# Performance work log

Hardware: AMD Instinct MI355X
Metric: run time of the kernel (lower is better)

Reference implementation:

```python
import jax, jax.numpy as jnp
import numpy as np

K = 9          # neighbors
DIL = 1        # dilation
BN_EPS = 1e-5

def _bn(x, g, b, m, v):
    # inference batchnorm over channel (last) dim
    return (x - m) * (g * jax.lax.rsqrt(v + BN_EPS)) + b

def setup_inputs() -> dict:
    key = jax.random.key(0)
    ks = jax.random.split(key, 4)
    B, C, H, W = 8, 192, 56, 56
    Ch = 384
    s = 0.02
    return {
        'x': jax.random.normal(ks[0], (B, C, H, W), jnp.float32),
        'fc1_w': jax.random.normal(ks[1], (C, C), jnp.float32) * s,
        'fc1_b': jnp.zeros((C,), jnp.float32),
        'bn1_g': jnp.ones((C,), jnp.float32), 'bn1_b': jnp.zeros((C,), jnp.float32),
        'bn1_m': jnp.zeros((C,), jnp.float32), 'bn1_v': jnp.ones((C,), jnp.float32),
        'gc_w': jax.random.normal(ks[2], (Ch, 2 * C), jnp.float32) * s,
        'gc_b': jnp.zeros((Ch,), jnp.float32),
        'bn2_g': jnp.ones((Ch,), jnp.float32), 'bn2_b': jnp.zeros((Ch,), jnp.float32),
        'bn2_m': jnp.zeros((Ch,), jnp.float32), 'bn2_v': jnp.ones((Ch,), jnp.float32),
        'fc2_w': jax.random.normal(ks[3], (C, Ch), jnp.float32) * s,
        'fc2_b': jnp.zeros((C,), jnp.float32),
        'bn3_g': jnp.ones((C,), jnp.float32), 'bn3_b': jnp.zeros((C,), jnp.float32),
        'bn3_m': jnp.zeros((C,), jnp.float32), 'bn3_v': jnp.ones((C,), jnp.float32),
    }

def reference(x, fc1_w, fc1_b, bn1_g, bn1_b, bn1_m, bn1_v,
              gc_w, gc_b, bn2_g, bn2_b, bn2_m, bn2_v,
              fc2_w, fc2_b, bn3_g, bn3_b, bn3_m, bn3_v):
    B, C, H, W = x.shape
    N = H * W
    xf = x.reshape(B, C, N).transpose(0, 2, 1)          # (B, N, C) nodes
    shortcut = xf
    # fc1: 1x1 conv + BN
    h = _bn(jnp.einsum('bnc,oc->bno', xf, fc1_w) + fc1_b, bn1_g, bn1_b, bn1_m, bn1_v)
    # dynamic KNN on L2-normalized features (ViG dense_knn_matrix)
    hn = h / jnp.maximum(jnp.linalg.norm(h, axis=-1, keepdims=True), 1e-12)
    sim = jnp.einsum('bnc,bmc->bnm', hn, hn)            # (B, N, N) cosine sim
    _, idx = jax.lax.top_k(sim, K * DIL)                # nearest (incl. self)
    idx = idx[..., ::DIL]                               # dilated neighbors (B,N,K)
    # gather neighbor features
    x_j = jax.vmap(lambda hb, ib: hb[ib])(h, idx)       # (B, N, K, C)
    x_i = h[:, :, None, :]                              # (B, N, 1, C)
    feat = jnp.concatenate([jnp.broadcast_to(x_i, x_j.shape), x_j - x_i], axis=-1)
    # EdgeConv: conv then max over neighbors
    e = jnp.einsum('bnke,oe->bnko', feat, gc_w) + gc_b  # (B, N, K, Ch)
    m = jnp.max(e, axis=2)                              # (B, N, Ch)
    m = jax.nn.gelu(_bn(m, bn2_g, bn2_b, bn2_m, bn2_v), approximate=False)
    # fc2: 1x1 conv + BN, residual
    out = _bn(jnp.einsum('bnh,oh->bno', m, fc2_w) + fc2_b, bn3_g, bn3_b, bn3_m, bn3_v)
    out = out + shortcut
    return out.transpose(0, 2, 1).reshape(B, C, H, W)
```

## Files before the change

kernel.cpp:

```cpp
#include <hip/hip_runtime.h>

#define BDIM 256
#define NB 8
#define NC 192
#define NN 3136
#define NCH 384
#define NK 9
#define NROW (NB * NN)

typedef __attribute__((ext_vector_type(8))) short short8;
typedef __attribute__((ext_vector_type(4))) float f32x4;

__device__ __forceinline__ unsigned short f2bf(float f) {
  union { float f; unsigned u; } x{f};
  unsigned r = x.u + 0x7fff + ((x.u >> 16) & 1);
  return (unsigned short)(r >> 16);
}

__device__ __forceinline__ float bf2f(unsigned u16) {
  union { unsigned u; float f; } x{u16 << 16};
  return x.f;
}

__device__ __forceinline__ unsigned umax_(unsigned a, unsigned b) { return a > b ? a : b; }
__device__ __forceinline__ unsigned umin_(unsigned a, unsigned b) { return a < b ? a : b; }
#define UMAX3(a, b, c) umax_(umax_((a), (b)), (c))
#define CXD(x, y)                      \
  {                                    \
    unsigned h_ = umax_(x, y);         \
    unsigned l_ = umin_(x, y);         \
    x = h_;                            \
    y = l_;                            \
  }

__device__ __forceinline__ unsigned simkey(float f, unsigned it) {
  union { float f; unsigned u; } x{f + 2.0f};
  return (x.u & 0xFFFFF000u) | it;
}

__device__ __forceinline__ void gload16(const char* g, char* l) {
  __builtin_amdgcn_global_load_lds(
      (const __attribute__((address_space(1))) unsigned int*)g,
      (__attribute__((address_space(3))) unsigned int*)l, 16, 0, 0);
}

__device__ __forceinline__ void stage_tile(const char* gbase, char* lbuf, int t) {
#pragma unroll
  for (int i = 0; i < 6; ++i) {
    int L = (i * 256 + t) * 16;
    int m = L / 384;
    int kb = L - m * 384;
    gload16(gbase + m * 384 + (kb ^ ((m & 7) << 4)), lbuf + L);
  }
}

__global__ __launch_bounds__(BDIM) void k0_convw(
    const float* __restrict__ gw, const float* __restrict__ f1w,
    const float* __restrict__ f2w, unsigned short* __restrict__ gcwb,
    unsigned short* __restrict__ fc1b, unsigned short* __restrict__ fc2b) {
  int i = (blockIdx.x * BDIM + threadIdx.x) * 4;
  const float* src;
  unsigned short* dst;
  if (i < 147456) {
    int o = i / NC, k = i - o * NC;
    src = gw + (size_t)(o < NCH ? o : o - NCH) * (2 * NC) + (o < NCH ? 0 : NC) + k;
    dst = gcwb + i;
  } else if (i < 184320) {
    int j = i - 147456;
    src = f1w + j;
    dst = fc1b + j;
  } else {
    int j = i - 184320;
    int o = j / NCH, k = j - o * NCH;
    int oc = o >> 6, om = o & 63;
    int kh = k / 192, km = k - kh * 192;
    src = f2w + j;
    dst = fc2b + ((size_t)((oc * 2 + kh) * 64 + om)) * 192 + km;
  }
  float4 v = *(const float4*)src;
  uint2 u;
  u.x = (unsigned)f2bf(v.x) | ((unsigned)f2bf(v.y) << 16);
  u.y = (unsigned)f2bf(v.z) | ((unsigned)f2bf(v.w) << 16);
  *(uint2*)dst = u;
}

__global__ __launch_bounds__(384) void k0b_params(
    const float* __restrict__ f1b, const float* __restrict__ g1,
    const float* __restrict__ b1, const float* __restrict__ m1,
    const float* __restrict__ v1, const float* __restrict__ gcb,
    const float* __restrict__ g2, const float* __restrict__ b2,
    const float* __restrict__ m2, const float* __restrict__ v2,
    const float* __restrict__ f2b, const float* __restrict__ g3,
    const float* __restrict__ b3, const float* __restrict__ m3,
    const float* __restrict__ v3, float* __restrict__ sc1,
    float* __restrict__ sh1, float* __restrict__ sc2, float* __restrict__ sh2,
    float* __restrict__ sc3, float* __restrict__ sh3) {
  int c = threadIdx.x;
  if (c < NC) {
    float s1 = g1[c] * rsqrtf(v1[c] + 1e-5f);
    sc1[c] = s1;
    sh1[c] = (f1b[c] - m1[c]) * s1 + b1[c];
    float s3 = g3[c] * rsqrtf(v3[c] + 1e-5f);
    sc3[c] = s3;
    sh3[c] = (f2b[c] - m3[c]) * s3 + b3[c];
  }
  float s2 = g2[c] * rsqrtf(v2[c] + 1e-5f);
  sc2[c] = s2;
  sh2[c] = (gcb[c] - m2[c]) * s2 + b2[c];
}

__global__ __launch_bounds__(BDIM) void k1_mfma(
    const float* __restrict__ x, const unsigned short* __restrict__ fc1b,
    const float* __restrict__ sc1, const float* __restrict__ sh1,
    unsigned short* __restrict__ hnb, float* __restrict__ normo) {
  __shared__ __align__(16) char abuf[2][24576];
  int t = threadIdx.x;
  int b = blockIdx.x / 49, n0 = (blockIdx.x % 49) * 64;
  int lane = t & 63, w = t >> 6;
  int l15 = lane & 15, l4 = lane >> 4;
  int n = n0 + w * 16 + l15;
  short8 bfr[6];
  {
    const float* xcol = x + (size_t)b * NC * NN + n;
#pragma unroll
    for (int ks = 0; ks < 6; ++ks) {
      union { short8 s; unsigned u[4]; } pk;
#pragma unroll
      for (int j = 0; j < 4; ++j) {
        float v0 = xcol[(size_t)(ks * 32 + l4 * 8 + 2 * j) * NN];
        float v1 = xcol[(size_t)(ks * 32 + l4 * 8 + 2 * j + 1) * NN];
        pk.u[j] = (unsigned)f2bf(v0) | ((unsigned)f2bf(v1) << 16);
      }
      bfr[ks] = pk.s;
    }
  }
  f32x4 acc[3][4];
#pragma unroll
  for (int oc = 0; oc < 3; ++oc)
#pragma unroll
    for (int sub = 0; sub < 4; ++sub) acc[oc][sub] = {0.f, 0.f, 0.f, 0.f};

  const char* wB = (const char*)fc1b;
  stage_tile(wB, abuf[0], t);
  __syncthreads();
  for (int oc = 0; oc < 3; ++oc) {
    int cur = oc & 1;
    if (oc < 2) stage_tile(wB + (size_t)(oc + 1) * 24576, abuf[cur ^ 1], t);
#pragma unroll
    for (int sub = 0; sub < 4; ++sub) {
      int r_ = sub * 16 + l15;
      int rbase = r_ * 384, sw = (r_ & 7) << 4;
#pragma unroll
      for (int ks = 0; ks < 6; ++ks) {
        short8 af = *(const short8*)&abuf[cur][rbase + ((ks * 64 + l4 * 16) ^ sw)];
        acc[oc][sub] = __builtin_amdgcn_mfma_f32_16x16x32_bf16(af, bfr[ks],
                                                               acc[oc][sub], 0, 0, 0);
      }
    }
    __syncthreads();
  }
  float p = 0.f;
#pragma unroll
  for (int oc = 0; oc < 3; ++oc)
#pragma unroll
    for (int sub = 0; sub < 4; ++sub) {
      int c4 = oc * 64 + sub * 16 + l4 * 4;
      float s_[4], h_[4];
      *(float4*)s_ = *(const float4*)&sc1[c4];
      *(float4*)h_ = *(const float4*)&sh1[c4];
#pragma unroll
      for (int r = 0; r < 4; ++r) {
        float v = acc[oc][sub][r] * s_[r] + h_[r];
        acc[oc][sub][r] = v;
        p += v * v;
      }
    }
  p += __shfl_xor(p, 16);
  p += __shfl_xor(p, 32);
  float nr = fmaxf(sqrtf(p), 1e-12f);
  float iv = 1.f / nr;
  if (l4 == 0) normo[(size_t)b * NN + n] = nr;
#pragma unroll
  for (int oc = 0; oc < 3; ++oc)
#pragma unroll
    for (int sub = 0; sub < 4; ++sub) {
      uint2 u;
      u.x = (unsigned)f2bf(acc[oc][sub][0] * iv) |
            ((unsigned)f2bf(acc[oc][sub][1] * iv) << 16);
      u.y = (unsigned)f2bf(acc[oc][sub][2] * iv) |
            ((unsigned)f2bf(acc[oc][sub][3] * iv) << 16);
      *(uint2*)&hnb[(size_t)(b * NN + n) * NC + oc * 64 + sub * 16 + l4 * 4] = u;
    }
}

__global__ __launch_bounds__(512) void k23_fused(
    const unsigned short* __restrict__ hnb, const float* __restrict__ norm,
    const unsigned short* __restrict__ gcwb, unsigned* __restrict__ candK,
    unsigned short* __restrict__ P, unsigned short* __restrict__ Q) {
  __shared__ __align__(16) char abuf[3][12288];
  int t = threadIdx.x;
  int bid = blockIdx.x;
  int b = bid & 7;
  int j = bid >> 3;
  int lane = t & 63, w = t >> 6;
  int l15 = lane & 15, l4 = lane >> 4;
  int wg = w & 3, sub = w >> 2;
  const unsigned short* hb = hnb + (size_t)b * NN * NC;

  int LA = t * 16;
  int mA = LA / 384, kbA = LA - mA * 384;
  int gA = mA * 384 + (kbA ^ ((mA & 7) << 4));
  int LB = (384 + t) * 16;
  int mB = LB / 384, kbB = LB - mB * 384;
  int gB = mB * 384 + (kbB ^ ((mB & 7) << 4));
  bool stg = (t < 384);
  int r_ = sub * 16 + l15;
  int rbase = r_ * 384, sw = (r_ & 7) << 4;
  int dso[6];
#pragma unroll
  for (int ks = 0; ks < 6; ++ks) dso[ks] = rbase + ((ks * 64 + l4 * 16) ^ sw);

  if (j % 5 != 4) {
    int idx2a = (j / 5) * 4 + (j % 5);
    int n0 = (idx2a >> 2) * 64;
    int seg = idx2a & 3;
    int mt0 = (98 * seg) / 4, mt1 = (98 * (seg + 1)) / 4;
    const char* hbB = (const char*)hb;

    short8 bfr[6];
    {
      const short8* brow =
          (const short8*)(hb + (size_t)(n0 + wg * 16 + l15) * NC + l4 * 8);
#pragma unroll
      for (int ks = 0; ks < 6; ++ks) bfr[ks] = brow[ks * 4];
    }
    unsigned tk[NK];
#pragma unroll
    for (int r = 0; r < NK; ++r) tk[r] = 0u;

    {
      const char* src = hbB + (size_t)mt0 * 12288;
      if (stg) { gload16(src + gA, abuf[0] + LA); gload16(src + gB, abuf[0] + LB); }
    }
    int nt = mt1 - mt0;
    int cur = 0;
    for (int ti = 0; ti < nt; ++ti) {
      int nxt = cur + 1 == 3 ? 0 : cur + 1;
      if (ti + 1 < nt) {
        const char* src = hbB + (size_t)(mt0 + ti + 1) * 12288;
        char* dl = &abuf[nxt][0];
        if (stg) { gload16(src + gA, dl + LA); gload16(src + gB, dl + LB); }
        asm volatile("s_waitcnt vmcnt(2)" ::: "memory");
      } else {
        asm volatile("s_waitcnt vmcnt(0)" ::: "memory");
      }
      __builtin_amdgcn_s_barrier();
      __builtin_amdgcn_sched_barrier(0);
      const char* lb = &abuf[cur][0];
      short8 af[6];
#pragma unroll
      for (int ks = 0; ks < 6; ++ks) af[ks] = *(const short8*)&lb[dso[ks]];
      f32x4 acc = {0.f, 0.f, 0.f, 0.f};
#pragma unroll
      for (int ks = 0; ks < 6; ++ks)
        acc = __builtin_amdgcn_mfma_f32_16x16x32_bf16(af[ks], bfr[ks], acc, 0, 0, 0);
      unsigned mknd = (unsigned)(4095 - ((mt0 + ti) * 32 + sub * 16 + l4 * 4));
      unsigned c0 = simkey(acc[0], mknd);
      unsigned c1 = simkey(acc[1], mknd - 1);
      unsigned c2 = simkey(acc[2], mknd - 2);
      unsigned c3 = simkey(acc[3], mknd - 3);
      CXD(c0, c1); CXD(c2, c3); CXD(c0, c2); CXD(c1, c3); CXD(c1, c2);
      tk[8] = UMAX3(UMAX3(tk[8], umin_(tk[7], c0), umin_(tk[6], c1)),
                    umin_(tk[5], c2), umin_(tk[4], c3));
      tk[7] = UMAX3(UMAX3(tk[7], umin_(tk[6], c0), umin_(tk[5], c1)),
                    umin_(tk[4], c2), umin_(tk[3], c3));
      tk[6] = UMAX3(UMAX3(tk[6], umin_(tk[5], c0), umin_(tk[4], c1)),
                    umin_(tk[3], c2), umin_(tk[2], c3));
      tk[5] = UMAX3(UMAX3(tk[5], umin_(tk[4], c0), umin_(tk[3], c1)),
                    umin_(tk[2], c2), umin_(tk[1], c3));
      tk[4] = UMAX3(UMAX3(tk[4], umin_(tk[3], c0), umin_(tk[2], c1)),
                    umin_(tk[1], c2), umin_(tk[0], c3));
      tk[3] = UMAX3(UMAX3(tk[3], c3, umin_(tk[2], c0)),
                    umin_(tk[1], c1), umin_(tk[0], c2));
      tk[2] = umax_(UMAX3(tk[2], c2, umin_(tk[1], c0)), umin_(tk[0], c1));
      tk[1] = UMAX3(tk[1], c1, umin_(tk[0], c0));
      tk[0] = umax_(tk[0], c0);
      cur = nxt;
    }
    __syncthreads();
    unsigned* mkeys = (unsigned*)&abuf[0][0];
    int rw = wg * 16 + l15;
#pragma unroll
    for (int r = 0; r < NK; ++r) mkeys[(rw * 8 + sub * 4 + l4) * NK + r] = tk[r];
    __syncthreads();
    if (t < 256) {
      int row = t >> 2, g = t & 3;
      unsigned* a = &mkeys[(row * 8 + g) * NK];
      const unsigned* c = &mkeys[(row * 8 + g + 4) * NK];
      unsigned best[NK];
#pragma unroll
      for (int r = 0; r < NK; ++r) best[r] = 0u;
#pragma unroll
      for (int s = 0; s < 2 * NK; ++s) {
        unsigned cur_k = s < NK ? a[s] : c[s - NK];
#pragma unroll
        for (int q = 0; q < NK; ++q) {
          unsigned hi = best[q] > cur_k ? best[q] : cur_k;
          unsigned lo = best[q] > cur_k ? cur_k : best[q];
          best[q] = hi;
          cur_k = lo;
        }
      }
#pragma unroll
      for (int r = 0; r < NK; ++r) a[r] = best[r];
    }
    __syncthreads();
    if (t < 64) {
      const unsigned* src = &mkeys[(t * 8) * NK];
      unsigned best[NK];
#pragma unroll
      for (int r = 0; r < NK; ++r) best[r] = 0u;
      for (int s = 0; s < 36; ++s) {
        unsigned cur_k = src[s];
#pragma unroll
        for (int q = 0; q < NK; ++q) {
          unsigned hi = best[q] > cur_k ? best[q] : cur_k;
          unsigned lo = best[q] > cur_k ? cur_k : best[q];
          best[q] = hi;
          cur_k = lo;
        }
      }
      size_t row = (size_t)b * NN + n0 + t;
#pragma unroll
      for (int r = 0; r < NK; ++r)
        candK[(size_t)(seg * NK + r) * NROW + row] = best[r];
    }
  } else {
    int jj = j / 5;
    int n0 = jj * 64;
    int n = n0 + wg * 16 + l15;
    short8 bfr[6];
    {
      const short8* brow = (const short8*)(hb + (size_t)n * NC + l4 * 8);
#pragma unroll
      for (int ks = 0; ks < 6; ++ks) bfr[ks] = brow[ks * 4];
    }
    float nrm = norm[(size_t)b * NN + n];
    size_t orow = (size_t)b * NN + n;
    const char* wB = (const char*)gcwb;

    if (stg) { gload16(wB + gA, abuf[0] + LA); gload16(wB + gB, abuf[0] + LB); }
    int cur = 0;
    for (int ch = 0; ch < 24; ++ch) {
      int nxt = cur + 1 == 3 ? 0 : cur + 1;
      if (ch < 23) {
        const char* src = wB + (size_t)(ch + 1) * 12288;
        char* dl = &abuf[nxt][0];
        if (stg) { gload16(src + gA, dl + LA); gload16(src + gB, dl + LB); }
        asm volatile("s_waitcnt vmcnt(3)" ::: "memory");
      } else {
        asm volatile("s_waitcnt vmcnt(0)" ::: "memory");
      }
      __builtin_amdgcn_s_barrier();
      __builtin_amdgcn_sched_barrier(0);
      const char* lb = &abuf[cur][0];
      f32x4 acc = {0.f, 0.f, 0.f, 0.f};
#pragma unroll
      for (int ks = 0; ks < 6; ++ks) {
        short8 af = *(const short8*)&lb[dso[ks]];
        acc = __builtin_amdgcn_mfma_f32_16x16x32_bf16(af, bfr[ks], acc, 0, 0, 0);
      }
      int o = ch * 32 + sub * 16 + l4 * 4;
      f32x4 st = acc * nrm;
      unsigned short* dst = (o < NCH) ? P : Q;
      int oo = (o < NCH) ? o : o - NCH;
      uint2 u;
      u.x = (unsigned)f2bf(st[0]) | ((unsigned)f2bf(st[1]) << 16);
      u.y = (unsigned)f2bf(st[2]) | ((unsigned)f2bf(st[3]) << 16);
      *(uint2*)&dst[orow * NCH + oo] = u;
      cur = nxt;
    }
  }
}

__global__ __launch_bounds__(BDIM) void k2b_merge(const unsigned* __restrict__ candK,
                                                  int* __restrict__ idxo) {
  int row = blockIdx.x * BDIM + threadIdx.x;
  unsigned tk[NK];
#pragma unroll
  for (int r = 0; r < NK; ++r) tk[r] = 0u;
  for (int s = 0; s < 4 * NK; ++s) {
    unsigned cur = candK[(size_t)s * NROW + row];
#pragma unroll
    for (int j = 0; j < NK; ++j) {
      unsigned hi = tk[j] > cur ? tk[j] : cur;
      unsigned lo = tk[j] > cur ? cur : tk[j];
      tk[j] = hi;
      cur = lo;
    }
  }
#pragma unroll
  for (int r = 0; r < NK; ++r)
    idxo[(size_t)row * NK + r] = 4095 - (int)(tk[r] & 4095u);
}

__global__ __launch_bounds__(BDIM) void k4_gathermax(
    const unsigned short* __restrict__ P, const unsigned short* __restrict__ Q,
    const int* __restrict__ idx, const float* __restrict__ sc2,
    const float* __restrict__ sh2, unsigned short* __restrict__ mbh) {
  int t = threadIdx.x;
  int lane = t & 63, wv = t >> 6;
  int b = blockIdx.x & 7;
  int n = (int)(blockIdx.x >> 3) * 4 + wv;
  size_t row = (size_t)b * NN + n;
  const int* ip = idx + row * NK;
  int id[NK];
#pragma unroll
  for (int k = 0; k < NK; ++k) id[k] = ip[k];
  const unsigned short* Qb = Q + (size_t)b * NN * NCH;
  const unsigned short* Pr = P + row * NCH;
  const unsigned short* Qr = Qb + (size_t)n * NCH;
#pragma unroll
  for (int j = 0; j < 3; ++j) {
    int o = j * 128 + lane * 2;
    float mx0 = -1e30f, mx1 = -1e30f;
#pragma unroll
    for (int k = 0; k < NK; ++k) {
      unsigned g = *(const unsigned*)&Qb[(size_t)id[k] * NCH + o];
      mx0 = fmaxf(mx0, bf2f(g & 0xffffu));
      mx1 = fmaxf(mx1, bf2f(g >> 16));
    }
    unsigned pv = *(const unsigned*)&Pr[o];
    unsigned qv = *(const unsigned*)&Qr[o];
    float2 ss = *(const float2*)&sc2[o];
    float2 hh = *(const float2*)&sh2[o];
    float e0 = bf2f(pv & 0xffffu) - bf2f(qv & 0xffffu) + mx0;
    float e1 = bf2f(pv >> 16) - bf2f(qv >> 16) + mx1;
    float y0 = e0 * ss.x + hh.x;
    float y1 = e1 * ss.y + hh.y;
    float ge0 = 0.5f * y0 * (1.f + erff(y0 * 0.70710678118654752f));
    float ge1 = 0.5f * y1 * (1.f + erff(y1 * 0.70710678118654752f));
    *(unsigned*)&mbh[row * NCH + o] =
        (unsigned)f2bf(ge0) | ((unsigned)f2bf(ge1) << 16);
  }
}

__global__ __launch_bounds__(BDIM) void k5_mfma(
    const unsigned short* __restrict__ mbh, const unsigned short* __restrict__ fc2b,
    const float* __restrict__ sc3, const float* __restrict__ sh3,
    const float* __restrict__ x, float* __restrict__ out) {
  __shared__ __align__(16) char abuf[2][24576];
  int t = threadIdx.x;
  int bid = blockIdx.x;
  int b = bid / 147;
  int rem = bid % 147;
  int n0 = (rem / 3) * 64;
  int oc = rem % 3;
  int lane = t & 63, w = t >> 6;
  int l15 = lane & 15, l4 = lane >> 4;
  int n = n0 + w * 16 + l15;
  short8 bfr[12];
  {
    const short8* brow = (const short8*)(mbh + (size_t)(b * NN + n) * NCH + l4 * 8);
#pragma unroll
    for (int kh = 0; kh < 2; ++kh)
#pragma unroll
      for (int ks = 0; ks < 6; ++ks) bfr[kh * 6 + ks] = brow[kh * 24 + ks * 4];
  }
  f32x4 acc[4];
#pragma unroll
  for (int sub = 0; sub < 4; ++sub) acc[sub] = {0.f, 0.f, 0.f, 0.f};

  const char* wt = (const char*)fc2b + (size_t)oc * 2 * 24576;
  stage_tile(wt, abuf[0], t);
  __syncthreads();
  for (int kh = 0; kh < 2; ++kh) {
    if (kh == 0) stage_tile(wt + 24576, abuf[1], t);
#pragma unroll
    for (int sub = 0; sub < 4; ++sub) {
      int r_ = sub * 16 + l15;
      int rbase = r_ * 384, sw = (r_ & 7) << 4;
#pragma unroll
      for (int ks = 0; ks < 6; ++ks) {
        short8 af = *(const short8*)&abuf[kh][rbase + ((ks * 64 + l4 * 16) ^ sw)];
        acc[sub] = __builtin_amdgcn_mfma_f32_16x16x32_bf16(af, bfr[kh * 6 + ks],
                                                           acc[sub], 0, 0, 0);
      }
    }
    __syncthreads();
  }
  const float* xb_ = x + (size_t)b * NC * NN;
  float* ob = out + (size_t)b * NC * NN;
#pragma unroll
  for (int sub = 0; sub < 4; ++sub) {
    int c4 = oc * 64 + sub * 16 + l4 * 4;
    float s_[4], h_[4];
    *(float4*)s_ = *(const float4*)&sc3[c4];
    *(float4*)h_ = *(const float4*)&sh3[c4];
#pragma unroll
    for (int r = 0; r < 4; ++r) {
      size_t off = (size_t)(c4 + r) * NN + n;
      ob[off] = acc[sub][r] * s_[r] + h_[r] + xb_[off];
    }
  }
}

extern "C" void kernel_launch(void* const* d_in, const int* in_sizes, int n_in,
                              void* d_out, int out_size, void* d_ws, size_t ws_size,
                              hipStream_t stream) {
  const float* x = (const float*)d_in[0];
  const float* fc1_w = (const float*)d_in[1];
  const float* fc1_b = (const float*)d_in[2];
  const float* bn1_g = (const float*)d_in[3];
  const float* bn1_b = (const float*)d_in[4];
  const float* bn1_m = (const float*)d_in[5];
  const float* bn1_v = (const float*)d_in[6];
  const float* gc_w = (const float*)d_in[7];
  const float* gc_b = (const float*)d_in[8];
  const float* bn2_g = (const float*)d_in[9];
  const float* bn2_b = (const float*)d_in[10];
  const float* bn2_m = (const float*)d_in[11];
  const float* bn2_v = (const float*)d_in[12];
  const float* fc2_w = (const float*)d_in[13];
  const float* fc2_b = (const float*)d_in[14];
  const float* bn3_g = (const float*)d_in[15];
  const float* bn3_b = (const float*)d_in[16];
  const float* bn3_m = (const float*)d_in[17];
  const float* bn3_v = (const float*)d_in[18];

  size_t nrow = (size_t)NROW;
  size_t npq = (size_t)NB * NN * NCH;
  size_t nhb = (size_t)NB * NN * NC;
  unsigned short* Pb = (unsigned short*)d_ws;
  unsigned short* Qb = Pb + npq;
  unsigned short* mbh = Qb + npq;
  float* norm = (float*)(mbh + npq);
  int* idx = (int*)(norm + nrow);
  unsigned short* hnb = (unsigned short*)(idx + nrow * NK);
  unsigned short* gcwb = hnb + nhb;
  unsigned short* fc1b = gcwb + 768 * NC;
  unsigned short* fc2b = fc1b + NC * NC;
  unsigned* candK = (unsigned*)(fc2b + NC * NCH);
  float* sc1 = (float*)(candK + 4 * NK * nrow);
  float* sh1 = sc1 + NC;
  float* sc2 = sh1 + NC;
  float* sh2 = sc2 + NCH;
  float* sc3 = sh2 + NCH;
  float* sh3 = sc3 + NC;

  k0_convw<<<252, BDIM, 0, stream>>>(gc_w, fc1_w, fc2_w, gcwb, fc1b, fc2b);
  k0b_params<<<1, 384, 0, stream>>>(fc1_b, bn1_g, bn1_b, bn1_m, bn1_v, gc_b,
                                    bn2_g, bn2_b, bn2_m, bn2_v, fc2_b, bn3_g,
                                    bn3_b, bn3_m, bn3_v, sc1, sh1, sc2, sh2,
                                    sc3, sh3);
  k1_mfma<<<NB * 49, BDIM, 0, stream>>>(x, fc1b, sc1, sh1, hnb, norm);
  k23_fused<<<NB * 245, 512, 0, stream>>>(hnb, norm, gcwb, candK, Pb, Qb);
  k2b_merge<<<NROW / BDIM, BDIM, 0, stream>>>(candK, idx);
  k4_gathermax<<<(NB * NN) / 4, BDIM, 0, stream>>>(Pb, Qb, idx, sc2, sh2, mbh);
  k5_mfma<<<NB * 147, BDIM, 0, stream>>>(mbh, fc2b, sc3, sh3, x, (float*)d_out);
}
```

Before: 144.8 us.

## Retile KNN similarity loop to 64-row candidate tiles with double-buffering

In the KNN branch of the fused kernel, each wave now computes two 16-column query blocks against a shared A fragment. Each step stages 64 candidate rows (24KB) instead of 32, and the 3-deep ring buffer becomes a double buffer with an extra trailing barrier. This halves the number of loop iterations and barriers and reuses each LDS A-fragment load across two MFMAs. In exchange it raises register pressure (two top-k arrays and two B fragment sets), and the reduction now merges 16 partial lists per row instead of 8.

```diff
diff --git a/kernel.cpp b/kernel.cpp
--- a/kernel.cpp
+++ b/kernel.cpp
@@ -32,6 +32,25 @@
     x = h_;                            \
     y = l_;                            \
   }
+#define SEL94(TK, a0, a1, a2, a3)                                          \
+  {                                                                        \
+    CXD(a0, a1); CXD(a2, a3); CXD(a0, a2); CXD(a1, a3); CXD(a1, a2);       \
+    TK[8] = UMAX3(UMAX3(TK[8], umin_(TK[7], a0), umin_(TK[6], a1)),        \
+                  umin_(TK[5], a2), umin_(TK[4], a3));                     \
+    TK[7] = UMAX3(UMAX3(TK[7], umin_(TK[6], a0), umin_(TK[5], a1)),        \
+                  umin_(TK[4], a2), umin_(TK[3], a3));                     \
+    TK[6] = UMAX3(UMAX3(TK[6], umin_(TK[5], a0), umin_(TK[4], a1)),        \
+                  umin_(TK[3], a2), umin_(TK[2], a3));                     \
+    TK[5] = UMAX3(UMAX3(TK[5], umin_(TK[4], a0), umin_(TK[3], a1)),        \
+                  umin_(TK[2], a2), umin_(TK[1], a3));                     \
+    TK[4] = UMAX3(UMAX3(TK[4], umin_(TK[3], a0), umin_(TK[2], a1)),        \
+                  umin_(TK[1], a2), umin_(TK[0], a3));                     \
+    TK[3] = UMAX3(UMAX3(TK[3], a3, umin_(TK[2], a0)),                      \
+                  umin_(TK[1], a1), umin_(TK[0], a2));                     \
+    TK[2] = umax_(UMAX3(TK[2], a2, umin_(TK[1], a0)), umin_(TK[0], a1));   \
+    TK[1] = UMAX3(TK[1], a1, umin_(TK[0], a0));                            \
+    TK[0] = umax_(TK[0], a0);                                              \
+  }
 
 __device__ __forceinline__ unsigned simkey(float f, unsigned it) {
   union { float f; unsigned u; } x{f + 2.0f};
@@ -48,6 +67,16 @@
 #pragma unroll
   for (int i = 0; i < 6; ++i) {
     int L = (i * 256 + t) * 16;
+    int m = L / 384;
+    int kb = L - m * 384;
+    gload16(gbase + m * 384 + (kb ^ ((m & 7) << 4)), lbuf + L);
+  }
+}
+
+__device__ __forceinline__ void stage64_512(const char* gbase, char* lbuf, int t) {
+#pragma unroll
+  for (int i = 0; i < 3; ++i) {
+    int L = (i * 512 + t) * 16;
     int m = L / 384;
     int kb = L - m * 384;
     gload16(gbase + m * 384 + (kb ^ ((m & 7) << 4)), lbuf + L);
@@ -197,117 +226,106 @@
     const unsigned short* __restrict__ hnb, const float* __restrict__ norm,
     const unsigned short* __restrict__ gcwb, unsigned* __restrict__ candK,
     unsigned short* __restrict__ P, unsigned short* __restrict__ Q) {
-  __shared__ __align__(16) char abuf[3][12288];
+  __shared__ __align__(16) char abuf[49152];
   int t = threadIdx.x;
   int bid = blockIdx.x;
   int b = bid & 7;
   int j = bid >> 3;
   int lane = t & 63, w = t >> 6;
   int l15 = lane & 15, l4 = lane >> 4;
-  int wg = w & 3, sub = w >> 2;
   const unsigned short* hb = hnb + (size_t)b * NN * NC;
-
-  int LA = t * 16;
-  int mA = LA / 384, kbA = LA - mA * 384;
-  int gA = mA * 384 + (kbA ^ ((mA & 7) << 4));
-  int LB = (384 + t) * 16;
-  int mB = LB / 384, kbB = LB - mB * 384;
-  int gB = mB * 384 + (kbB ^ ((mB & 7) << 4));
-  bool stg = (t < 384);
-  int r_ = sub * 16 + l15;
-  int rbase = r_ * 384, sw = (r_ & 7) << 4;
-  int dso[6];
-#pragma unroll
-  for (int ks = 0; ks < 6; ++ks) dso[ks] = rbase + ((ks * 64 + l4 * 16) ^ sw);
 
   if (j % 5 != 4) {
     int idx2a = (j / 5) * 4 + (j % 5);
     int n0 = (idx2a >> 2) * 64;
     int seg = idx2a & 3;
-    int mt0 = (98 * seg) / 4, mt1 = (98 * (seg + 1)) / 4;
+    int mt0 = (49 * seg) / 4, mt1 = (49 * (seg + 1)) / 4;
     const char* hbB = (const char*)hb;
-
-    short8 bfr[6];
+    int wgp = w & 1, sub = w >> 1;
+
+    short8 bfrA[6], bfrB[6];
     {
-      const short8* brow =
-          (const short8*)(hb + (size_t)(n0 + wg * 16 + l15) * NC + l4 * 8);
-#pragma unroll
-      for (int ks = 0; ks < 6; ++ks) bfr[ks] = brow[ks * 4];
-    }
-    unsigned tk[NK];
-#pragma unroll
-    for (int r = 0; r < NK; ++r) tk[r] = 0u;
-
-    {
-      const char* src = hbB + (size_t)mt0 * 12288;
-      if (stg) { gload16(src + gA, abuf[0] + LA); gload16(src + gB, abuf[0] + LB); }
-    }
+      const short8* ra =
+          (const short8*)(hb + (size_t)(n0 + wgp * 32 + l15) * NC + l4 * 8);
+      const short8* rb =
+          (const short8*)(hb + (size_t)(n0 + wgp * 32 + 16 + l15) * NC + l4 * 8);
+#pragma unroll
+      for (int ks = 0; ks < 6; ++ks) { bfrA[ks] = ra[ks * 4]; bfrB[ks] = rb[ks * 4]; }
+    }
+    int r_ = sub * 16 + l15;
+    int rbase = r_ * 384, sw = (r_ & 7) << 4;
+    int dso[6];
+#pragma unroll
+    for (int ks = 0; ks < 6; ++ks) dso[ks] = rbase + ((ks * 64 + l4 * 16) ^ sw);
+
+    unsigned tkA[NK], tkB[NK];
+#pragma unroll
+    for (int r = 0; r < NK; ++r) { tkA[r] = 0u; tkB[r] = 0u; }
+
+    stage64_512(hbB + (size_t)mt0 * 24576, abuf, t);
     int nt = mt1 - mt0;
     int cur = 0;
     for (int ti = 0; ti < nt; ++ti) {
-      int nxt = cur + 1 == 3 ? 0 : cur + 1;
       if (ti + 1 < nt) {
-        const char* src = hbB + (size_t)(mt0 + ti + 1) * 12288;
-        char* dl = &abuf[nxt][0];
-        if (stg) { gload16(src + gA, dl + LA); gload16(src + gB, dl + LB); }
-        asm volatile("s_waitcnt vmcnt(2)" ::: "memory");
+        stage64_512(hbB + (size_t)(mt0 + ti + 1) * 24576, abuf + (cur ^ 1) * 24576, t);
+        asm volatile("s_waitcnt vmcnt(3)" ::: "memory");
       } else {
         asm volatile("s_waitcnt vmcnt(0)" ::: "memory");
       }
       __builtin_amdgcn_s_barrier();
       __builtin_amdgcn_sched_barrier(0);
-      const char* lb = &abuf[cur][0];
+      const char* lb = abuf + cur * 24576;
       short8 af[6];
 #pragma unroll
       for (int ks = 0; ks < 6; ++ks) af[ks] = *(const short8*)&lb[dso[ks]];
-      f32x4 acc = {0.f, 0.f, 0.f, 0.f};
-#pragma unroll
-      for (int ks = 0; ks < 6; ++ks)
-        acc = __builtin_amdgcn_mfma_f32_16x16x32_bf16(af[ks], bfr[ks], acc, 0, 0, 0);
-      unsigned mknd = (unsigned)(4095 - ((mt0 + ti) * 32 + sub * 16 + l4 * 4));
-      unsigned c0 = simkey(acc[0], mknd);
-      unsigned c1 = simkey(acc[1], mknd - 1);
-      unsigned c2 = simkey(acc[2], mknd - 2);
-      unsigned c3 = simkey(acc[3], mknd - 3);
-      CXD(c0, c1); CXD(c2, c3); CXD(c0, c2); CXD(c1, c3); CXD(c1, c2);
-      tk[8] = UMAX3(UMAX3(tk[8], umin_(tk[7], c0), umin_(tk[6], c1)),
-                    umin_(tk[5], c2), umin_(tk[4], c3));
-      tk[7] = UMAX3(UMAX3(tk[7], umin_(tk[6], c0), umin_(tk[5], c1)),
-                    umin_(tk[4], c2), umin_(tk[3], c3));
-      tk[6] = UMAX3(UMAX3(tk[6], umin_(tk[5], c0), umin_(tk[4], c1)),
-                    umin_(tk[3], c2), umin_(tk[2], c3));
-      tk[5] = UMAX3(UMAX3(tk[5], umin_(tk[4], c0), umin_(tk[3], c1)),
-                    umin_(tk[2], c2), umin_(tk[1], c3));
-      tk[4] = UMAX3(UMAX3(tk[4], umin_(tk[3], c0), umin_(tk[2], c1)),
-                    umin_(tk[1], c2), umin_(tk[0], c3));
-      tk[3] = UMAX3(UMAX3(tk[3], c3, umin_(tk[2], c0)),
-                    umin_(tk[1], c1), umin_(tk[0], c2));
-      tk[2] = umax_(UMAX3(tk[2], c2, umin_(tk[1], c0)), umin_(tk[0], c1));
-      tk[1] = UMAX3(tk[1], c1, umin_(tk[0], c0));
-      tk[0] = umax_(tk[0], c0);
-      cur = nxt;
-    }
-    __syncthreads();
-    unsigned* mkeys = (unsigned*)&abuf[0][0];
-    int rw = wg * 16 + l15;
-#pragma unroll
-    for (int r = 0; r < NK; ++r) mkeys[(rw * 8 + sub * 4 + l4) * NK + r] = tk[r];
+      f32x4 accA = {0.f, 0.f, 0.f, 0.f};
+      f32x4 accB = {0.f, 0.f, 0.f, 0.f};
+#pragma unroll
+      for (int ks = 0; ks < 6; ++ks) {
+        accA = __builtin_amdgcn_mfma_f32_16x16x32_bf16(af[ks], bfrA[ks], accA, 0, 0, 0);
+        accB = __builtin_amdgcn_mfma_f32_16x16x32_bf16(af[ks], bfrB[ks], accB, 0, 0, 0);
+      }
+      unsigned mknd = (unsigned)(4095 - ((mt0 + ti) * 64 + sub * 16 + l4 * 4));
+      {
+        unsigned c0 = simkey(accA[0], mknd);
+        unsigned c1 = simkey(accA[1], mknd - 1);
+        unsigned c2 = simkey(accA[2], mknd - 2);
+        unsigned c3 = simkey(accA[3], mknd - 3);
+        SEL94(tkA, c0, c1, c2, c3);
+      }
+      {
+        unsigned c0 = simkey(accB[0], mknd);
+        unsigned c1 = simkey(accB[1], mknd - 1);
+        unsigned c2 = simkey(accB[2], mknd - 2);
+        unsigned c3 = simkey(accB[3], mknd - 3);
+        SEL94(tkB, c0, c1, c2, c3);
+      }
+      __builtin_amdgcn_sched_barrier(0);
+      __builtin_amdgcn_s_barrier();
+      cur ^= 1;
+    }
+    unsigned* mkeys = (unsigned*)abuf;
+    int slot = sub * 4 + l4;
+    int rowA = wgp * 32 + l15, rowB = wgp * 32 + 16 + l15;
+#pragma unroll
+    for (int r = 0; r < NK; ++r) {
+      mkeys[(rowA * 16 + slot) * NK + r] = tkA[r];
+      mkeys[(rowB * 16 + slot) * NK + r] = tkB[r];
+    }
     __syncthreads();
     if (t < 256) {
-      int row = t >> 2, g = t & 3;
-      unsigned* a = &mkeys[(row * 8 + g) * NK];
-      const unsigned* c = &mkeys[(row * 8 + g + 4) * NK];
+      int row = t >> 2, q = t & 3;
+      unsigned* a = &mkeys[(row * 16 + q * 4) * NK];
       unsigned best[NK];
 #pragma unroll
       for (int r = 0; r < NK; ++r) best[r] = 0u;
-#pragma unroll
-      for (int s = 0; s < 2 * NK; ++s) {
-        unsigned cur_k = s < NK ? a[s] : c[s - NK];
-#pragma unroll
-        for (int q = 0; q < NK; ++q) {
-          unsigned hi = best[q] > cur_k ? best[q] : cur_k;
-          unsigned lo = best[q] > cur_k ? cur_k : best[q];
-          best[q] = hi;
+      for (int s = 0; s < 36; ++s) {
+        unsigned cur_k = a[s];
+#pragma unroll
+        for (int q2 = 0; q2 < NK; ++q2) {
+          unsigned hi = best[q2] > cur_k ? best[q2] : cur_k;
+          unsigned lo = best[q2] > cur_k ? cur_k : best[q2];
+          best[q2] = hi;
           cur_k = lo;
         }
       }
@@ -316,28 +334,31 @@
     }
     __syncthreads();
     if (t < 64) {
-      const unsigned* src = &mkeys[(t * 8) * NK];
+      const unsigned* base = &mkeys[t * 16 * NK];
       unsigned best[NK];
 #pragma unroll
       for (int r = 0; r < NK; ++r) best[r] = 0u;
-      for (int s = 0; s < 36; ++s) {
-        unsigned cur_k = src[s];
-#pragma unroll
-        for (int q = 0; q < NK; ++q) {
-          unsigned hi = best[q] > cur_k ? best[q] : cur_k;
-          unsigned lo = best[q] > cur_k ? cur_k : best[q];
-          best[q] = hi;
-          cur_k = lo;
+#pragma unroll
+      for (int q = 0; q < 4; ++q)
+        for (int s = 0; s < NK; ++s) {
+          unsigned cur_k = base[q * 36 + s];
+#pragma unroll
+          for (int q2 = 0; q2 < NK; ++q2) {
+            unsigned hi = best[q2] > cur_k ? best[q2] : cur_k;
+            unsigned lo = best[q2] > cur_k ? cur_k : best[q2];
+            best[q2] = hi;
+            cur_k = lo;
+          }
         }
-      }
-      size_t row = (size_t)b * NN + n0 + t;
+      size_t rowg = (size_t)b * NN + n0 + t;
 #pragma unroll
       for (int r = 0; r < NK; ++r)
-        candK[(size_t)(seg * NK + r) * NROW + row] = best[r];
+        candK[(size_t)(seg * NK + r) * NROW + rowg] = best[r];
     }
   } else {
     int jj = j / 5;
     int n0 = jj * 64;
+    int wg = w & 3, sub = w >> 2;
     int n = n0 + wg * 16 + l15;
     short8 bfr[6];
     {
@@ -349,13 +370,26 @@
     size_t orow = (size_t)b * NN + n;
     const char* wB = (const char*)gcwb;
 
-    if (stg) { gload16(wB + gA, abuf[0] + LA); gload16(wB + gB, abuf[0] + LB); }
+    int LA = t * 16;
+    int mA = LA / 384, kbA = LA - mA * 384;
+    int gA = mA * 384 + (kbA ^ ((mA & 7) << 4));
+    int LB = (384 + t) * 16;
+    int mB = LB / 384, kbB = LB - mB * 384;
+    int gB = mB * 384 + (kbB ^ ((mB & 7) << 4));
+    bool stg = (t < 384);
+    int r_ = sub * 16 + l15;
+    int rbase = r_ * 384, sw = (r_ & 7) << 4;
+    int dso[6];
+#pragma unroll
+    for (int ks = 0; ks < 6; ++ks) dso[ks] = rbase + ((ks * 64 + l4 * 16) ^ sw);
+
+    if (stg) { gload16(wB + gA, abuf + LA); gload16(wB + gB, abuf + LB); }
     int cur = 0;
     for (int ch = 0; ch < 24; ++ch) {
       int nxt = cur + 1 == 3 ? 0 : cur + 1;
       if (ch < 23) {
         const char* src = wB + (size_t)(ch + 1) * 12288;
-        char* dl = &abuf[nxt][0];
+        char* dl = abuf + nxt * 12288;
         if (stg) { gload16(src + gA, dl + LA); gload16(src + gB, dl + LB); }
         asm volatile("s_waitcnt vmcnt(3)" ::: "memory");
       } else {
@@ -363,7 +397,7 @@
       }
       __builtin_amdgcn_s_barrier();
       __builtin_amdgcn_sched_barrier(0);
-      const char* lb = &abuf[cur][0];
+      const char* lb = abuf + cur * 12288;
       f32x4 acc = {0.f, 0.f, 0.f, 0.f};
 #pragma unroll
       for (int ks = 0; ks < 6; ++ks) {
```

New measurement: 164.1 us. 13.3% more time.
